# Optimization experiments

Measured on AMD Instinct MI355X. Metric: run time of the kernel, lower is better.

The kernel has to match this reference:

```python
import jax, jax.numpy as jnp
import numpy as np

N_HEAD = 16
NEG = -10000.0


def setup_inputs() -> dict:
    key = jax.random.key(0)
    k1, k2, k3 = jax.random.split(key, 3)
    B, S, NX = 2, 2048, 1024
    x = jax.random.normal(k1, (B, S, NX), dtype=jnp.float32)
    # Conv1D weights: y = x @ W + b (HF Conv1D stores weight as [in, out])
    w_attn = jax.random.normal(k2, (NX, 3 * NX), dtype=jnp.float32) * 0.02
    b_attn = jnp.zeros((3 * NX,), dtype=jnp.float32)
    w_proj = jax.random.normal(k3, (NX, NX), dtype=jnp.float32) * 0.02
    b_proj = jnp.zeros((NX,), dtype=jnp.float32)
    return {"x": x, "w_attn": w_attn, "b_attn": b_attn,
            "w_proj": w_proj, "b_proj": b_proj}


def reference(x, w_attn, b_attn, w_proj, b_proj):
    B, S, NX = x.shape
    H = N_HEAD
    D = NX // H  # head dim
    qkv = x @ w_attn + b_attn                      # [B, S, 3*NX]
    q, k, v = jnp.split(qkv, 3, axis=-1)
    # split heads -> [B, H, S, D]
    q = q.reshape(B, S, H, D).transpose(0, 2, 1, 3)
    k = k.reshape(B, S, H, D).transpose(0, 2, 1, 3)
    v = v.reshape(B, S, H, D).transpose(0, 2, 1, 3)
    # scores [B, H, S, S], scaled (scale=True)
    w = jnp.einsum('bhqd,bhkd->bhqk', q, k) / jnp.sqrt(jnp.asarray(D, x.dtype))
    # causal additive mask exactly as the torch code: w*b + NEG*(1-b)
    bias = jnp.tril(jnp.ones((S, S), dtype=x.dtype))[None, None]  # [1,1,S,S]
    w = w * bias + NEG * (1.0 - bias)
    w = jax.nn.softmax(w, axis=-1)
    a = jnp.einsum('bhqk,bhkd->bhqd', w, v)        # [B, H, S, D]
    a = a.transpose(0, 2, 1, 3).reshape(B, S, NX)  # merge heads
    return a @ w_proj + b_proj
```

## Files before the change

kernel.cpp:

```cpp
#include <hip/hip_runtime.h>
#include <cstdint>
#include <cstddef>


typedef __bf16 bf16;
typedef __bf16 bf16x8 __attribute__((ext_vector_type(8)));
typedef __bf16 bf16x4 __attribute__((ext_vector_type(4)));
typedef float f32x4 __attribute__((ext_vector_type(4)));
typedef float f32x16 __attribute__((ext_vector_type(16)));

#define MFMA16(a, b, c) __builtin_amdgcn_mfma_f32_16x16x32_bf16(a, b, c, 0, 0, 0)
#define MFMA32(a, b, c) __builtin_amdgcn_mfma_f32_32x32x16_bf16(a, b, c, 0, 0, 0)

typedef const __attribute__((address_space(1))) void* gas_ptr;
typedef __attribute__((address_space(3))) void* las_ptr;
__device__ __forceinline__ void async16(const void* g, void* l) {
    __builtin_amdgcn_global_load_lds((gas_ptr)g, (las_ptr)l, 16, 0, 0);
}
__device__ __forceinline__ float exp2f_fast(float x) { return __builtin_amdgcn_exp2f(x); }
__device__ __forceinline__ uint32_t pkbf(float a, float b) {
    union { bf16 x[2]; uint32_t u; } t;
    t.x[0] = (bf16)a; t.x[1] = (bf16)b;
    return t.u;
}

__global__ __launch_bounds__(256) void prep_kernel(const float* __restrict__ x, bf16* __restrict__ xb,
                                                   const float* __restrict__ wa, bf16* __restrict__ wTa,
                                                   const float* __restrict__ wp, bf16* __restrict__ wTp) {
    __shared__ float tile[32][33];
    const int bid = blockIdx.x, tid = threadIdx.x;
    if (bid < 4096) {
        int i = (bid * 256 + tid) * 4;
        float4 v = *reinterpret_cast<const float4*>(x + i);
        bf16x4 o;
        o[0] = (bf16)v.x; o[1] = (bf16)v.y; o[2] = (bf16)v.z; o[3] = (bf16)v.w;
        *reinterpret_cast<bf16x4*>(xb + i) = o;
        return;
    }
    const float* in; bf16* out; int N, t;
    if (bid < 7168) { t = bid - 4096; in = wa; out = wTa; N = 3072; }
    else            { t = bid - 7168; in = wp; out = wTp; N = 1024; }
    const int K = 1024;
    int bx = t % (N >> 5), by = t / (N >> 5);
    int n0 = bx * 32, k0 = by * 32, tx = tid & 31, ty = tid >> 5;
#pragma unroll
    for (int i = 0; i < 32; i += 8)
        tile[ty + i][tx] = in[(size_t)(k0 + ty + i) * N + n0 + tx];
    __syncthreads();
#pragma unroll
    for (int i = 0; i < 32; i += 8)
        out[(size_t)(n0 + ty + i) * K + k0 + tx] = (bf16)tile[tx][ty + i];
}

template <int OUT_BF16>
__global__ __launch_bounds__(256) void gemm_kernel(const bf16* __restrict__ A,
                                                   const bf16* __restrict__ Bt,
                                                   const float* __restrict__ bias,
                                                   void* __restrict__ Cout,
                                                   int M, int N, int K) {
    __shared__ bf16 Alds[2][128 * 32];
    __shared__ bf16 Blds[2][128 * 32];
    const int tid = threadIdx.x;
    const int w = tid >> 6, l = tid & 63;
    const int lane16 = l & 15, quad = l >> 4;
    const int wr = w >> 1, wc = w & 1;

    const int nwg = gridDim.x * gridDim.y;
    const int lin = blockIdx.x + gridDim.x * blockIdx.y;
    const int q8 = nwg >> 3;
    const int swz = (lin & 7) * q8 + (lin >> 3);
    const int bx = swz % gridDim.x, by = swz / gridDim.x;
    const int row0 = by * 128, col0 = bx * 128;

    int grs[2], gks[2];
#pragma unroll
    for (int c = 0; c < 2; ++c) {
        int idx = c * 256 + tid;
        int R = idx >> 3, pos = idx & 7;
        int pos2 = pos ^ (R & 7);
        grs[c] = 2 * R + (pos2 >> 2);
        gks[c] = (pos2 & 3) * 8;
    }

    f32x4 zero4 = {0.f, 0.f, 0.f, 0.f};
    f32x4 acc[4][4];
#pragma unroll
    for (int i = 0; i < 4; ++i)
#pragma unroll
        for (int j = 0; j < 4; ++j) acc[i][j] = zero4;

    auto stage = [&](int buf, int k0) {
#pragma unroll
        for (int c = 0; c < 2; ++c) {
            int idx = c * 256 + tid;
            async16(A + (size_t)(row0 + grs[c]) * K + k0 + gks[c], &Alds[buf][idx * 8]);
            async16(Bt + (size_t)(col0 + grs[c]) * K + k0 + gks[c], &Blds[buf][idx * 8]);
        }
    };

    stage(0, 0);
    const int niter = K >> 5;
    for (int it = 0; it < niter; ++it) {
        const int cur = it & 1;
        __syncthreads();
        if (it + 1 < niter) stage(cur ^ 1, (it + 1) << 5);
        bf16x8 af[4], bfr[4];
#pragma unroll
        for (int i = 0; i < 4; ++i) {
            int gra = 64 * wr + 16 * i + lane16;
            int Ra = gra >> 1;
            int pa = ((gra & 1) * 4 + quad) ^ (Ra & 7);
            af[i] = *reinterpret_cast<const bf16x8*>(&Alds[cur][Ra * 64 + pa * 8]);
            int grb = 64 * wc + 16 * i + lane16;
            int Rb = grb >> 1;
            int pb = ((grb & 1) * 4 + quad) ^ (Rb & 7);
            bfr[i] = *reinterpret_cast<const bf16x8*>(&Blds[cur][Rb * 64 + pb * 8]);
        }
#pragma unroll
        for (int i = 0; i < 4; ++i)
#pragma unroll
            for (int j = 0; j < 4; ++j) acc[i][j] = MFMA16(af[i], bfr[j], acc[i][j]);
    }

#pragma unroll
    for (int i = 0; i < 4; ++i)
#pragma unroll
        for (int j = 0; j < 4; ++j)
#pragma unroll
            for (int r = 0; r < 4; ++r) {
                int row = row0 + 64 * wr + 16 * i + quad * 4 + r;
                int col = col0 + 64 * wc + 16 * j + lane16;
                float v = acc[i][j][r] + bias[col];
                if (OUT_BF16)
                    reinterpret_cast<bf16*>(Cout)[(size_t)row * N + col] = (bf16)v;
                else
                    reinterpret_cast<float*>(Cout)[(size_t)row * N + col] = v;
            }
}

template <int OUT_BF16>
__global__ __launch_bounds__(256) void gemm64k_kernel(const bf16* __restrict__ A,
                                                      const bf16* __restrict__ Bt,
                                                      const float* __restrict__ bias,
                                                      void* __restrict__ Cout,
                                                      int M, int N, int K) {
    __shared__ bf16 Alds[2][64 * 64];
    __shared__ bf16 Blds[2][128 * 64];
    const int tid = threadIdx.x;
    const int w = tid >> 6, l = tid & 63;
    const int lane16 = l & 15, quad = l >> 4;
    const int wr = w >> 1, wc = w & 1;
    const int row0 = blockIdx.y * 64, col0 = blockIdx.x * 128;

    f32x4 zero4 = {0.f, 0.f, 0.f, 0.f};
    f32x4 acc[2][4];
#pragma unroll
    for (int i = 0; i < 2; ++i)
#pragma unroll
        for (int j = 0; j < 4; ++j) acc[i][j] = zero4;

    auto stage = [&](int buf, int k0) {
#pragma unroll
        for (int c = 0; c < 2; ++c) {
            int idx = c * 256 + tid;
            int r = idx >> 3, cc = idx & 7, gc = cc ^ (r & 7);
            async16(A + (size_t)(row0 + r) * K + k0 + gc * 8, &Alds[buf][idx * 8]);
        }
#pragma unroll
        for (int c = 0; c < 4; ++c) {
            int idx = c * 256 + tid;
            int r = idx >> 3, cc = idx & 7, gc = cc ^ (r & 7);
            async16(Bt + (size_t)(col0 + r) * K + k0 + gc * 8, &Blds[buf][idx * 8]);
        }
    };

    stage(0, 0);
    const int niter = K >> 6;
    for (int it = 0; it < niter; ++it) {
        const int cur = it & 1;
        __syncthreads();
        if (it + 1 < niter) stage(cur ^ 1, (it + 1) << 6);
        bf16x8 af[2][2], bfr[4][2];
#pragma unroll
        for (int i = 0; i < 2; ++i) {
            int r = 32 * wr + 16 * i + lane16;
#pragma unroll
            for (int ks = 0; ks < 2; ++ks) {
                int cc = (quad + 4 * ks) ^ (r & 7);
                af[i][ks] = *reinterpret_cast<const bf16x8*>(&Alds[cur][r * 64 + cc * 8]);
            }
        }
#pragma unroll
        for (int j = 0; j < 4; ++j) {
            int r = 64 * wc + 16 * j + lane16;
#pragma unroll
            for (int ks = 0; ks < 2; ++ks) {
                int cc = (quad + 4 * ks) ^ (r & 7);
                bfr[j][ks] = *reinterpret_cast<const bf16x8*>(&Blds[cur][r * 64 + cc * 8]);
            }
        }
#pragma unroll
        for (int ks = 0; ks < 2; ++ks)
#pragma unroll
            for (int i = 0; i < 2; ++i)
#pragma unroll
                for (int j = 0; j < 4; ++j) acc[i][j] = MFMA16(af[i][ks], bfr[j][ks], acc[i][j]);
    }

#pragma unroll
    for (int i = 0; i < 2; ++i)
#pragma unroll
        for (int j = 0; j < 4; ++j)
#pragma unroll
            for (int r = 0; r < 4; ++r) {
                int row = row0 + 32 * wr + 16 * i + quad * 4 + r;
                int col = col0 + 64 * wc + 16 * j + lane16;
                float v = acc[i][j][r] + bias[col];
                if (OUT_BF16)
                    reinterpret_cast<bf16*>(Cout)[(size_t)row * N + col] = (bf16)v;
                else
                    reinterpret_cast<float*>(Cout)[(size_t)row * N + col] = v;
            }
}

__global__ __launch_bounds__(256, 4) void attn_kernel(const bf16* __restrict__ qkv,
                                                      bf16* __restrict__ aout) {
    const int S = 2048;
    const int bh = blockIdx.x;
    const int b = bh >> 4, hd = bh & 15;
    const int rr = blockIdx.y >> 3, j = blockIdx.y & 7;
    const int qt = (rr == 0) ? (31 - j) : (rr == 1) ? (16 + j) : (rr == 2) ? (15 - j) : j;
    const int nkt = qt + 1;
    const int tid = threadIdx.x, w = tid >> 6, l = tid & 63;
    const int lane32 = l & 31, h = l >> 5;
    const int qh = w & 1, kh = w >> 1;

    __shared__ bf16 Klds[2][64 * 64];
    __shared__ bf16 Vt[2][64 * 64];
    __shared__ float Lbuf[2][2][32];

    const bf16* base = qkv + (size_t)b * S * 3072;
    const float qscale = 0.125f * 1.4426950408889634f;
    const float NEGs = -10000.0f * 1.4426950408889634f;

    bf16x8 qf[4];
    {
        const bf16* qp = base + (size_t)(qt * 64 + qh * 32 + lane32) * 3072 + hd * 64;
#pragma unroll
        for (int s = 0; s < 4; ++s) {
            bf16x8 t = *reinterpret_cast<const bf16x8*>(qp + s * 16 + h * 8);
#pragma unroll
            for (int jj = 0; jj < 8; ++jj) t[jj] = (bf16)((float)t[jj] * qscale);
            qf[s] = t;
        }
    }

    f32x16 oacc[2];
#pragma unroll
    for (int dt = 0; dt < 2; ++dt)
#pragma unroll
        for (int i = 0; i < 16; ++i) oacc[dt][i] = 0.f;
    float lsum = 0.f;

    const int kr = tid >> 3, kcc = tid & 7;
    const int vp = tid & 31, vd = (tid >> 5) * 8;
    bf16x8 kreg0, kreg1, vreg0, vreg1;
    auto load_tile = [&](int kt) {
        const bf16* tb = base + (size_t)(kt * 64) * 3072;
        kreg0 = *reinterpret_cast<const bf16x8*>(tb + (size_t)kr * 3072 + 1024 + hd * 64 + kcc * 8);
        kreg1 = *reinterpret_cast<const bf16x8*>(tb + (size_t)(32 + kr) * 3072 + 1024 + hd * 64 + kcc * 8);
        vreg0 = *reinterpret_cast<const bf16x8*>(tb + (size_t)(2 * vp) * 3072 + 2048 + hd * 64 + vd);
        vreg1 = *reinterpret_cast<const bf16x8*>(tb + (size_t)(2 * vp + 1) * 3072 + 2048 + hd * 64 + vd);
    };
    auto write_KV = [&](int buf) {
        bf16* Kb = &Klds[buf][0];
        bf16* Vb = &Vt[buf][0];
        const int kchunk = kcc ^ (kr & 7);
        *reinterpret_cast<bf16x8*>(&Kb[kr * 64 + kchunk * 8]) = kreg0;
        *reinterpret_cast<bf16x8*>(&Kb[(32 + kr) * 64 + kchunk * 8]) = kreg1;
#pragma unroll
        for (int jj = 0; jj < 8; ++jj) {
            int row = vd + jj;
            union { bf16 h2v[2]; uint32_t u; } pk;
            pk.h2v[0] = vreg0[jj]; pk.h2v[1] = vreg1[jj];
            int idx = row * 64 + (((vp >> 2) ^ (row & 7)) * 8) + (vp & 3) * 2;
            *reinterpret_cast<uint32_t*>(&Vb[idx]) = pk.u;
        }
    };

    load_tile(0);
    write_KV(0);
    if (nkt > 1) load_tile(1);
    __syncthreads();

    const int krow = kh * 32 + lane32;
    for (int kt = 0; kt < nkt; ++kt) {
        const int p = kt & 1;
        if (kt + 1 < nkt) write_KV(p ^ 1);

        f32x16 st;
#pragma unroll
        for (int i = 0; i < 16; ++i) st[i] = 0.f;
        __builtin_amdgcn_s_setprio(1);
#pragma unroll
        for (int s = 0; s < 4; ++s) {
            int ch = (2 * s + h) ^ (krow & 7);
            bf16x8 kf = *reinterpret_cast<const bf16x8*>(&Klds[p][krow * 64 + ch * 8]);
            st = MFMA32(kf, qf[s], st);
        }
        __builtin_amdgcn_s_setprio(0);

        if (kt + 2 < nkt) load_tile(kt + 2);

        if (kt == qt) {
            const int q = qh * 32 + lane32;
#pragma unroll
            for (int reg = 0; reg < 16; ++reg) {
                int kloc = kh * 32 + 4 * h + (reg & 3) + 8 * (reg >> 2);
                if (kloc > q) st[reg] = NEGs;
            }
        }

        uint32_t wpk[4][2];
        float rs = 0.f;
#pragma unroll
        for (int g = 0; g < 4; ++g) {
            float p0 = exp2f_fast(st[4 * g + 0]);
            float p1 = exp2f_fast(st[4 * g + 1]);
            float p2 = exp2f_fast(st[4 * g + 2]);
            float p3 = exp2f_fast(st[4 * g + 3]);
            rs += (p0 + p1) + (p2 + p3);
            wpk[g][0] = pkbf(p0, p1);
            wpk[g][1] = pkbf(p2, p3);
        }
        lsum += rs;

        uint32_t opk[4][2];
#pragma unroll
        for (int g = 0; g < 4; ++g) {
            opk[g][0] = (uint32_t)__shfl_xor((int)wpk[g][0], 32, 64);
            opk[g][1] = (uint32_t)__shfl_xor((int)wpk[g][1], 32, 64);
        }

        bf16x8 pf[2];
#pragma unroll
        for (int s2 = 0; s2 < 2; ++s2) {
            union { uint32_t u[4]; bf16x8 v; } pu;
            const int g0 = 2 * s2, g1 = 2 * s2 + 1;
            pu.u[0] = h ? opk[g1][0] : wpk[g0][0];
            pu.u[1] = h ? opk[g1][1] : wpk[g0][1];
            pu.u[2] = h ? wpk[g1][0] : opk[g0][0];
            pu.u[3] = h ? wpk[g1][1] : opk[g0][1];
            pf[s2] = pu.v;
        }

        __builtin_amdgcn_s_setprio(1);
#pragma unroll
        for (int dt = 0; dt < 2; ++dt) {
            int vrow = dt * 32 + lane32;
#pragma unroll
            for (int s2 = 0; s2 < 2; ++s2) {
                int kc = (4 * kh + 2 * s2 + h) ^ (vrow & 7);
                bf16x8 vf = *reinterpret_cast<const bf16x8*>(&Vt[p][vrow * 64 + kc * 8]);
                oacc[dt] = MFMA32(pf[s2], vf, oacc[dt]);
            }
        }
        __builtin_amdgcn_s_setprio(0);

        __syncthreads();
    }

    lsum += __shfl_xor(lsum, 32, 64);
    if (l < 32) Lbuf[kh][qh][lane32] = lsum;

    float* Obuf = reinterpret_cast<float*>(&Klds[0][0]);
    if (kh == 1) {
#pragma unroll
        for (int dt = 0; dt < 2; ++dt)
#pragma unroll
            for (int reg = 0; reg < 16; ++reg) {
                int qrow = (reg & 3) + 8 * (reg >> 2) + 4 * h;
                Obuf[(qh * 32 + qrow) * 64 + dt * 32 + lane32] = oacc[dt][reg];
            }
    }
    __syncthreads();

    if (kh == 0) {
        float linv[16];
#pragma unroll
        for (int reg = 0; reg < 16; ++reg) {
            int qrow = (reg & 3) + 8 * (reg >> 2) + 4 * h;
            linv[reg] = 1.0f / (Lbuf[0][qh][qrow] + Lbuf[1][qh][qrow]);
        }
#pragma unroll
        for (int dt = 0; dt < 2; ++dt)
#pragma unroll
            for (int reg = 0; reg < 16; ++reg) {
                int qrow = (reg & 3) + 8 * (reg >> 2) + 4 * h;
                float v = (oacc[dt][reg] + Obuf[(qh * 32 + qrow) * 64 + dt * 32 + lane32]) * linv[reg];
                aout[(size_t)(b * S + qt * 64 + qh * 32 + qrow) * 1024 + hd * 64 + dt * 32 + lane32] =
                    (bf16)v;
            }
    }
}

extern "C" void kernel_launch(void* const* d_in, const int* in_sizes, int n_in,
                              void* d_out, int out_size, void* d_ws, size_t ws_size,
                              hipStream_t stream) {
    const float* x      = (const float*)d_in[0];
    const float* w_attn = (const float*)d_in[1];
    const float* b_attn = (const float*)d_in[2];
    const float* w_proj = (const float*)d_in[3];
    const float* b_proj = (const float*)d_in[4];
    float* out = (float*)d_out;
    char* ws = (char*)d_ws;

    const int Mtok = 4096, NX = 1024, N3 = 3072;
    bf16* xb   = (bf16*)(ws);
    bf16* wTa  = (bf16*)(ws + ((size_t)8 << 20));
    bf16* wTp  = (bf16*)(ws + ((size_t)14 << 20));
    bf16* qkv  = (bf16*)(ws + ((size_t)16 << 20));
    bf16* abuf = (bf16*)(ws + ((size_t)40 << 20));

    prep_kernel<<<dim3(8192), 256, 0, stream>>>(x, xb, w_attn, wTa, w_proj, wTp);
    gemm_kernel<1><<<dim3(N3 / 128, Mtok / 128), 256, 0, stream>>>(xb, wTa, b_attn, qkv, Mtok, N3, NX);
    attn_kernel<<<dim3(32, 32), 256, 0, stream>>>(qkv, abuf);
    gemm64k_kernel<0><<<dim3(NX / 128, Mtok / 64), 256, 0, stream>>>(abuf, wTp, b_proj, out, Mtok, NX, NX);
}
```

Baseline: 168.5 us.

## Replace QKV GEMM with 256x256 tiled, 4-stage pipelined 512-thread kernel

Replaces the 128x128 double-buffered QKV projection GEMM with a 256x256 tile kernel using 8 waves, a 4-slot LDS ring with loads issued two tiles ahead, explicit vmcnt/lgkmcnt waits, barriers and setprio around MFMA bursts. The goal is to raise arithmetic intensity per block and overlap global loads with MFMA work. The trade-off is far fewer blocks (192), which may underfill the GPU, plus 128 KB of LDS per block.

```diff
diff --git a/kernel.cpp b/kernel.cpp
--- a/kernel.cpp
+++ b/kernel.cpp
@@ -23,6 +23,11 @@
     t.x[0] = (bf16)a; t.x[1] = (bf16)b;
     return t.u;
 }
+
+#define WAITVM4()   asm volatile("s_waitcnt vmcnt(4)" ::: "memory")
+#define WAITVM0()   asm volatile("s_waitcnt vmcnt(0)" ::: "memory")
+#define WAITLGKM0() asm volatile("s_waitcnt lgkmcnt(0)" ::: "memory")
+#define SCHEDB()    __builtin_amdgcn_sched_barrier(0)
 
 __global__ __launch_bounds__(256) void prep_kernel(const float* __restrict__ x, bf16* __restrict__ xb,
                                                    const float* __restrict__ wa, bf16* __restrict__ wTa,
@@ -52,89 +57,117 @@
         out[(size_t)(n0 + ty + i) * K + k0 + tx] = (bf16)tile[tx][ty + i];
 }
 
-template <int OUT_BF16>
-__global__ __launch_bounds__(256) void gemm_kernel(const bf16* __restrict__ A,
-                                                   const bf16* __restrict__ Bt,
-                                                   const float* __restrict__ bias,
-                                                   void* __restrict__ Cout,
-                                                   int M, int N, int K) {
-    __shared__ bf16 Alds[2][128 * 32];
-    __shared__ bf16 Blds[2][128 * 32];
+__global__ __launch_bounds__(512, 2) void gemm256_kernel(const bf16* __restrict__ A,
+                                                         const bf16* __restrict__ Bt,
+                                                         const float* __restrict__ bias,
+                                                         bf16* __restrict__ Cout,
+                                                         int M, int N, int K) {
+    __shared__ bf16 lds[4][2][8192];
     const int tid = threadIdx.x;
     const int w = tid >> 6, l = tid & 63;
     const int lane16 = l & 15, quad = l >> 4;
-    const int wr = w >> 1, wc = w & 1;
+    const int wm = w >> 2, wn = w & 3;
 
     const int nwg = gridDim.x * gridDim.y;
     const int lin = blockIdx.x + gridDim.x * blockIdx.y;
     const int q8 = nwg >> 3;
     const int swz = (lin & 7) * q8 + (lin >> 3);
     const int bx = swz % gridDim.x, by = swz / gridDim.x;
-    const int row0 = by * 128, col0 = bx * 128;
-
-    int grs[2], gks[2];
-#pragma unroll
-    for (int c = 0; c < 2; ++c) {
-        int idx = c * 256 + tid;
-        int R = idx >> 3, pos = idx & 7;
-        int pos2 = pos ^ (R & 7);
-        grs[c] = 2 * R + (pos2 >> 2);
-        gks[c] = (pos2 & 3) * 8;
-    }
+    const int row0 = by * 256, col0 = bx * 256;
+
+    const int sR = tid >> 3, sposr = tid & 7;
+    const int spos2 = sposr ^ (sR & 7);
+    const int sr2 = 2 * sR + (spos2 >> 2);
+    const int sgk = (spos2 & 3) * 8;
+    auto stageA = [&](int slot, int tile, int h) {
+        async16(A + (size_t)(row0 + h * 128 + sr2) * K + (tile << 5) + sgk,
+                &lds[slot][0][h * 4096 + tid * 8]);
+    };
+    auto stageB = [&](int slot, int tile, int h) {
+        async16(Bt + (size_t)(col0 + h * 128 + sr2) * K + (tile << 5) + sgk,
+                &lds[slot][1][h * 4096 + tid * 8]);
+    };
+
+    const int fpos = (((lane16 & 1) << 2) + quad) ^ (lane16 >> 1);
+    const int fbA = wm * 4096 + (lane16 >> 1) * 64 + fpos * 8;
+    const int fbB = wn * 2048 + (lane16 >> 1) * 64 + fpos * 8;
 
     f32x4 zero4 = {0.f, 0.f, 0.f, 0.f};
-    f32x4 acc[4][4];
-#pragma unroll
-    for (int i = 0; i < 4; ++i)
+    f32x4 acc[8][4];
+#pragma unroll
+    for (int i = 0; i < 8; ++i)
 #pragma unroll
         for (int j = 0; j < 4; ++j) acc[i][j] = zero4;
 
-    auto stage = [&](int buf, int k0) {
-#pragma unroll
-        for (int c = 0; c < 2; ++c) {
-            int idx = c * 256 + tid;
-            async16(A + (size_t)(row0 + grs[c]) * K + k0 + gks[c], &Alds[buf][idx * 8]);
-            async16(Bt + (size_t)(col0 + grs[c]) * K + k0 + gks[c], &Blds[buf][idx * 8]);
-        }
-    };
-
-    stage(0, 0);
-    const int niter = K >> 5;
-    for (int it = 0; it < niter; ++it) {
-        const int cur = it & 1;
-        __syncthreads();
-        if (it + 1 < niter) stage(cur ^ 1, (it + 1) << 5);
-        bf16x8 af[4], bfr[4];
-#pragma unroll
-        for (int i = 0; i < 4; ++i) {
-            int gra = 64 * wr + 16 * i + lane16;
-            int Ra = gra >> 1;
-            int pa = ((gra & 1) * 4 + quad) ^ (Ra & 7);
-            af[i] = *reinterpret_cast<const bf16x8*>(&Alds[cur][Ra * 64 + pa * 8]);
-            int grb = 64 * wc + 16 * i + lane16;
-            int Rb = grb >> 1;
-            int pb = ((grb & 1) * 4 + quad) ^ (Rb & 7);
-            bfr[i] = *reinterpret_cast<const bf16x8*>(&Blds[cur][Rb * 64 + pb * 8]);
-        }
+#pragma unroll
+    for (int h = 0; h < 2; ++h) { stageA(0, 0, h); }
+#pragma unroll
+    for (int h = 0; h < 2; ++h) { stageB(0, 0, h); }
+#pragma unroll
+    for (int h = 0; h < 2; ++h) { stageA(1, 1, h); }
+#pragma unroll
+    for (int h = 0; h < 2; ++h) { stageB(1, 1, h); }
+    WAITVM4();
+    SCHEDB();
+    __builtin_amdgcn_s_barrier();
+
+    const int ntiles = K >> 5;
+    for (int t = 0; t < ntiles; ++t) {
+        const int slot = t & 3;
+        const int ps = (t + 2) & 3;
+        const bool pre = (t + 2) < ntiles;
+        const bf16* Ap = &lds[slot][0][0];
+        const bf16* Bp = &lds[slot][1][0];
+
+        bf16x8 bfr[4], af[4];
+#pragma unroll
+        for (int jn = 0; jn < 4; ++jn)
+            bfr[jn] = *reinterpret_cast<const bf16x8*>(&Bp[fbB + jn * 512]);
 #pragma unroll
         for (int i = 0; i < 4; ++i)
-#pragma unroll
-            for (int j = 0; j < 4; ++j) acc[i][j] = MFMA16(af[i], bfr[j], acc[i][j]);
-    }
-
-#pragma unroll
-    for (int i = 0; i < 4; ++i)
-#pragma unroll
-        for (int j = 0; j < 4; ++j)
+            af[i] = *reinterpret_cast<const bf16x8*>(&Ap[fbA + i * 512]);
+        if (pre) { stageA(ps, t + 2, 0); stageA(ps, t + 2, 1); }
+        SCHEDB();
+        __builtin_amdgcn_s_barrier();
+        WAITLGKM0();
+        SCHEDB();
+        __builtin_amdgcn_s_setprio(1);
+#pragma unroll
+        for (int i = 0; i < 4; ++i)
+#pragma unroll
+            for (int jn = 0; jn < 4; ++jn) acc[i][jn] = MFMA16(af[i], bfr[jn], acc[i][jn]);
+        __builtin_amdgcn_s_setprio(0);
+        SCHEDB();
+        __builtin_amdgcn_s_barrier();
+
+#pragma unroll
+        for (int i = 0; i < 4; ++i)
+            af[i] = *reinterpret_cast<const bf16x8*>(&Ap[fbA + (4 + i) * 512]);
+        if (pre) { stageB(ps, t + 2, 0); stageB(ps, t + 2, 1); }
+        SCHEDB();
+        __builtin_amdgcn_s_barrier();
+        WAITLGKM0();
+        SCHEDB();
+        __builtin_amdgcn_s_setprio(1);
+#pragma unroll
+        for (int i = 0; i < 4; ++i)
+#pragma unroll
+            for (int jn = 0; jn < 4; ++jn) acc[4 + i][jn] = MFMA16(af[i], bfr[jn], acc[4 + i][jn]);
+        __builtin_amdgcn_s_setprio(0);
+        if (pre) { WAITVM4(); } else { WAITVM0(); }
+        SCHEDB();
+        __builtin_amdgcn_s_barrier();
+    }
+
+#pragma unroll
+    for (int i = 0; i < 8; ++i)
+#pragma unroll
+        for (int jn = 0; jn < 4; ++jn)
 #pragma unroll
             for (int r = 0; r < 4; ++r) {
-                int row = row0 + 64 * wr + 16 * i + quad * 4 + r;
-                int col = col0 + 64 * wc + 16 * j + lane16;
-                float v = acc[i][j][r] + bias[col];
-                if (OUT_BF16)
-                    reinterpret_cast<bf16*>(Cout)[(size_t)row * N + col] = (bf16)v;
-                else
-                    reinterpret_cast<float*>(Cout)[(size_t)row * N + col] = v;
+                int row = row0 + wm * 128 + i * 16 + quad * 4 + r;
+                int col = col0 + wn * 64 + jn * 16 + lane16;
+                Cout[(size_t)row * N + col] = (bf16)(acc[i][jn][r] + bias[col]);
             }
 }
 
@@ -423,7 +456,7 @@
     bf16* abuf = (bf16*)(ws + ((size_t)40 << 20));
 
     prep_kernel<<<dim3(8192), 256, 0, stream>>>(x, xb, w_attn, wTa, w_proj, wTp);
-    gemm_kernel<1><<<dim3(N3 / 128, Mtok / 128), 256, 0, stream>>>(xb, wTa, b_attn, qkv, Mtok, N3, NX);
+    gemm256_kernel<<<dim3(N3 / 256, Mtok / 256), 512, 0, stream>>>(xb, wTa, b_attn, qkv, Mtok, N3, NX);
     attn_kernel<<<dim3(32, 32), 256, 0, stream>>>(qkv, abuf);
     gemm64k_kernel<0><<<dim3(NX / 128, Mtok / 64), 256, 0, stream>>>(abuf, wTp, b_proj, out, Mtok, NX, NX);
 }
```

Result: no change. 170.3 us (+1.0%).
